# Kernel optimization log

Measured on AMD Instinct MI355X. Metric: run time of the kernel, lower is better.

Reference implementation:

```python
import jax, jax.numpy as jnp
import numpy as np

B, L, V, D = 512, 41, 4, 64        # batch, seq_len=41 (hard-coded in source), vocab=DNA, d_model=64
NL, DI, N, DTR, K = 3, 128, 16, 4, 4  # n_layer, d_inner=2*D, d_state, dt_rank=ceil(D/16), d_conv
NS = 3  # three parallel stacks (layers1/2/3)


def setup_inputs() -> dict:
    key = jax.random.key(0)
    ks = jax.random.split(key, 16)
    s = 0.02
    nrm = lambda k, sh: jax.random.normal(k, sh, jnp.float32) * s
    A_log = jnp.log(jnp.arange(1, N + 1, dtype=jnp.float32))  # S4D-real init
    return {
        "input_ids": jax.random.randint(ks[0], (B, L), 0, V),
        "embedding": nrm(ks[1], (V, D)),
        # per-stack, per-layer Mamba block params, stacked [NS, NL, ...]
        "in_proj": nrm(ks[2], (NS, NL, D, 2 * DI)),
        "conv_w": nrm(ks[3], (NS, NL, DI, 1, K)),
        "conv_b": jnp.zeros((NS, NL, DI), jnp.float32),
        "x_proj": nrm(ks[4], (NS, NL, DI, DTR + 2 * N)),
        "dt_w": nrm(ks[5], (NS, NL, DTR, DI)),
        "dt_b": jnp.full((NS, NL, DI), -2.0, jnp.float32),
        "A_log": jnp.broadcast_to(A_log, (NS, NL, DI, N)) + 0.0,
        "Dp": jnp.ones((NS, NL, DI), jnp.float32),
        "out_proj": nrm(ks[6], (NS, NL, DI, D)),
        "norm_w": jnp.ones((NS, NL, D), jnp.float32),
        "norm_f_w": jnp.ones((D,), jnp.float32),
        "fusion_w": jnp.zeros((NS,), jnp.float32),  # softmax-weighted fusion of the 3 representations
        # LastDense MLP head: 64*41 -> 384 -> 16 -> 1 (dropout is eval-mode identity)
        "W1": nrm(ks[7], (D * L, 384)), "b1": jnp.zeros((384,), jnp.float32),
        "W2": nrm(ks[8], (384, 16)), "b2": jnp.zeros((16,), jnp.float32),
        "W3": nrm(ks[9], (16, 1)), "b3": jnp.zeros((1,), jnp.float32),
    }


def rmsnorm(x, w, eps=1e-5):
    return x * jax.lax.rsqrt(jnp.mean(x * x, axis=-1, keepdims=True) + eps) * w


def silu(x):
    return x * jax.nn.sigmoid(x)


def mamba_block(x, ip, cw, cb, xp, dw, db, al, dp, op):
    # x: [B, L, D]
    bsz = x.shape[0]
    u, res = jnp.split(x @ ip, 2, axis=-1)  # each [B, L, DI]
    # causal depthwise conv1d (torch padding=3 then [..., :L] == left-pad K-1)
    uc = jax.lax.conv_general_dilated(
        u.transpose(0, 2, 1), cw, window_strides=(1,), padding=[(K - 1, 0)],
        feature_group_count=DI, dimension_numbers=("NCH", "OIH", "NCH"))
    u = silu((uc + cb[None, :, None]).transpose(0, 2, 1))  # [B, L, DI]
    dbl = u @ xp  # [B, L, DTR+2N]
    dt = jax.nn.softplus(dbl[..., :DTR] @ dw + db)           # [B, L, DI]
    Bm = dbl[..., DTR:DTR + N]                               # [B, L, N]
    C = dbl[..., DTR + N:]                                   # [B, L, N]
    A = -jnp.exp(al)                                         # [DI, N]
    dA = jnp.exp(dt[..., None] * A)                          # [B, L, DI, N]
    dBu = dt[..., None] * Bm[:, :, None, :] * u[..., None]   # [B, L, DI, N]

    def step(h, xs):
        dA_t, dBu_t, C_t = xs
        h = dA_t * h + dBu_t                                 # [B, DI, N]
        return h, jnp.einsum("bdn,bn->bd", h, C_t)

    h0 = jnp.zeros((bsz, DI, N), x.dtype)
    _, ys = jax.lax.scan(step, h0, (dA.transpose(1, 0, 2, 3), dBu.transpose(1, 0, 2, 3), C.transpose(1, 0, 2)))
    y = ys.transpose(1, 0, 2) + u * dp                       # [B, L, DI]
    return (y * silu(res)) @ op                              # [B, L, D]


def _forward(input_ids, embedding, in_proj, conv_w, conv_b, x_proj, dt_w, dt_b,
             A_log, Dp, out_proj, norm_w, norm_f_w, fusion_w, W1, b1, W2, b2, W3, b3):
    emb = embedding[input_ids]  # [B, L, D]

    def run_stack(ip, cw, cb, xp, dw, db, al, dp, op, nw):
        x = emb
        for i in range(NL):  # residual: x + MambaBlock(RMSNorm(x))
            x = x + mamba_block(rmsnorm(x, nw[i]), ip[i], cw[i], cb[i], xp[i], dw[i], db[i], al[i], dp[i], op[i])
        return x

    stack_out = jax.vmap(run_stack)(in_proj, conv_w, conv_b, x_proj, dt_w, dt_b,
                                    A_log, Dp, out_proj, norm_w)  # [NS, B, L, D]
    stack_out = rmsnorm(stack_out, norm_f_w)  # final norm_f per stack
    fused = jnp.einsum("s,sbld->bld", jax.nn.softmax(fusion_w), stack_out)  # fusion of 3 reps
    flat = fused.reshape(fused.shape[0], L * D)
    h = jax.nn.relu(flat @ W1 + b1)
    h = jax.nn.relu(h @ W2 + b2)
    logits = (h @ W3 + b3)[:, 0]
    return jax.nn.sigmoid(logits)  # [B]


def reference(input_ids, embedding, in_proj, conv_w, conv_b, x_proj, dt_w, dt_b,
              A_log, Dp, out_proj, norm_w, norm_f_w, fusion_w, W1, b1, W2, b2, W3, b3):
    return _forward(input_ids, embedding, in_proj, conv_w, conv_b, x_proj, dt_w, dt_b,
                    A_log, Dp, out_proj, norm_w, norm_f_w, fusion_w, W1, b1, W2, b2, W3, b3)
```

## Files before the change

### kernel.cpp

```cpp
#include <hip/hip_runtime.h>
#include <hip/hip_bf16.h>
#include <math.h>

#define Bq  512
#define Lq  41
#define Vq  4
#define Dq  64
#define NLq 3
#define DIq 128
#define Nq  16
#define DTRq 4
#define Kq  4
#define NSq 3
#define H1q 384
#define H2q 16
#define FLATq (Lq*Dq)

typedef __attribute__((ext_vector_type(8))) short frag8;
typedef __attribute__((ext_vector_type(4))) float f32x4;

__device__ __forceinline__ float b2f(unsigned short u) {
    union { float f; unsigned int i; } v; v.i = ((unsigned int)u) << 16; return v.f;
}
__device__ __forceinline__ unsigned short f2b_rne(float f) {
    union { float f; unsigned int i; } v; v.f = f;
    unsigned int x = v.i;
    return (unsigned short)((x + 0x7fffu + ((x >> 16) & 1u)) >> 16);
}
__device__ __forceinline__ unsigned short f2b_tr(float f) {
    union { float f; unsigned int i; } v; v.f = f;
    return (unsigned short)(v.i >> 16);
}
__device__ __forceinline__ float fast_rcp(float x) { return __builtin_amdgcn_rcpf(x); }

__global__ __launch_bounds__(256) void prep_kernel(const float* __restrict__ W1,
                                                   const float* __restrict__ in_proj,
                                                   const float* __restrict__ x_proj,
                                                   const float* __restrict__ out_proj,
                                                   unsigned short* __restrict__ W1b,
                                                   unsigned short* __restrict__ Wb_in,
                                                   unsigned short* __restrict__ xp_b,
                                                   unsigned short* __restrict__ op_b) {
    const int bx = blockIdx.x;
    if (bx < 246) {
        __shared__ float t[64][65];
        const int k0 = (bx / 6) * 64, n0 = (bx % 6) * 64;
        for (int idx = threadIdx.x; idx < 4096; idx += 256) {
            int kr = idx >> 6, nc = idx & 63;
            t[kr][nc] = W1[(size_t)(k0 + kr) * H1q + n0 + nc];
        }
        __syncthreads();
        for (int idx = threadIdx.x; idx < 4096; idx += 256) {
            int nr = idx >> 6, kc = idx & 63;
            W1b[(size_t)(n0 + nr) * FLATq + k0 + kc] = f2b_rne(t[kc][nr]);
        }
        return;
    }
    int idx = (bx - 246) * 256 + threadIdx.x;
    if (idx < 9*256*64) {
        int sl = idx >> 14, rem = idx & 16383;
        int n = rem >> 6, k = rem & 63;
        Wb_in[idx] = f2b_rne(in_proj[(size_t)sl*16384 + k*256 + n]);
    } else if (idx < 9*256*64 + 9*48*128) {
        int i2 = idx - 9*256*64;
        int sl = i2 / 6144, rem = i2 % 6144;
        int c = rem >> 7, k = rem & 127;
        float v = (c < 36) ? x_proj[(size_t)sl*(128*36) + k*36 + c] : 0.f;
        xp_b[i2] = f2b_rne(v);
    } else if (idx < 9*256*64 + 9*48*128 + 9*64*128) {
        int i3 = idx - (9*256*64 + 9*48*128);
        int sl = i3 >> 13, rem = i3 & 8191;
        int n = rem >> 7, k = rem & 127;
        op_b[i3] = f2b_rne(out_proj[(size_t)sl*8192 + k*64 + n]);
    }
}

__global__ __launch_bounds__(256, 4) void mamba_stack(
    unsigned short* __restrict__ Xn,
    const int* __restrict__ ids,
    const float* __restrict__ emb,
    const unsigned short* __restrict__ Wb_in,
    const float* __restrict__ conv_w,
    const float* __restrict__ conv_b,
    const unsigned short* __restrict__ xp_b,
    const float* __restrict__ dt_w,
    const float* __restrict__ dt_b,
    const float* __restrict__ A_log,
    const float* __restrict__ Dp,
    const unsigned short* __restrict__ op_b,
    const float* __restrict__ norm_w,
    const float* __restrict__ norm_f_w,
    const float* __restrict__ fusion_w)
{
    const int b = blockIdx.x, s = blockIdx.y, tid = threadIdx.x;
    const int wave = tid >> 6, lane = tid & 63;
    const int nl = lane & 15, quad = lane >> 4;

    __shared__ float          xt  [Lq][64];
    __shared__ unsigned short u_lb[48][136];
    __shared__ unsigned short rs_lb[Lq][128];
    __shared__ __align__(16) char un_buf[6912];
    unsigned short (*xn_lb)[72] = (unsigned short(*)[72])un_buf;
    float          (*dbl_s)[40] = (float(*)[40])un_buf;

    for (int l = wave; l < Lq; l += 4) {
        int id = ids[b * Lq + l];
        xt[l][lane] = emb[id * Dq + lane];
    }

    for (int layer = 0; layer < NLq; ++layer) {
        const int sl = s * NLq + layer;

        {
            const float nwv = norm_w[(size_t)sl * Dq + lane];
            for (int l = wave; l < 48; l += 4) {
                if (l < Lq) {
                    float v  = xt[l][lane];
                    float ss = v * v;
                    #pragma unroll
                    for (int off = 32; off; off >>= 1) ss += __shfl_xor(ss, off, 64);
                    float scale = __builtin_amdgcn_rsqf(ss * (1.0f / Dq) + 1e-5f);
                    xn_lb[l][lane] = f2b_tr(v * scale * nwv);
                } else {
                    xn_lb[l][lane] = 0;
                }
            }
        }
        __syncthreads();

        {
            #pragma unroll
            for (int t = 0; t < 12; ++t) {
                const int id = wave * 12 + t;
                const int mt = id >> 4, nt = id & 15;
                const unsigned short* Wp = Wb_in + ((size_t)(sl * 256 + nt * 16 + nl)) * 64 + quad * 8;
                frag8 a0 = *(const frag8*)&xn_lb[mt * 16 + nl][quad * 8];
                frag8 a1 = *(const frag8*)&xn_lb[mt * 16 + nl][32 + quad * 8];
                frag8 b0 = *(const frag8*)&Wp[0];
                frag8 b1 = *(const frag8*)&Wp[32];
                f32x4 c = {0.f, 0.f, 0.f, 0.f};
                c = __builtin_amdgcn_mfma_f32_16x16x32_bf16(a0, b0, c, 0, 0, 0);
                c = __builtin_amdgcn_mfma_f32_16x16x32_bf16(a1, b1, c, 0, 0, 0);
                const int col = nt * 16 + nl;
                const int r0 = mt * 16 + quad * 4;
                if (col < DIq) {
                    #pragma unroll
                    for (int r = 0; r < 4; ++r) u_lb[r0 + r][col] = f2b_tr(c[r]);
                } else {
                    const int d = col - DIq;
                    #pragma unroll
                    for (int r = 0; r < 4; ++r) {
                        int row = r0 + r;
                        if (row < Lq) {
                            float v = c[r];
                            rs_lb[row][d] = f2b_tr(v * fast_rcp(1.f + __expf(-v)));
                        }
                    }
                }
            }
        }
        __syncthreads();

        {
            const float* cw = conv_w + (size_t)sl * (DIq * Kq);
            const int d = tid >> 1, half = tid & 1;
            const float c0 = cw[d*4+0], c1 = cw[d*4+1], c2 = cw[d*4+2], c3 = cw[d*4+3];
            const float cbv = conv_b[(size_t)sl * DIq + d];
            float w0 = 0.f, w1 = 0.f, w2 = 0.f;
            if (half) { w0 = b2f(u_lb[18][d]); w1 = b2f(u_lb[19][d]); w2 = b2f(u_lb[20][d]); }
            const int base = half ? 21 : 0;
            const int cnt  = half ? 20 : 21;
            for (int i = 0; i < cnt; ++i) {
                int l = base + i;
                float cur = b2f(u_lb[l][d]);
                float a = fmaf(w0, c0, fmaf(w1, c1, fmaf(w2, c2, fmaf(cur, c3, cbv))));
                u_lb[l][d] = f2b_tr(a * fast_rcp(1.f + __expf(-a)));
                w0 = w1; w1 = w2; w2 = cur;
            }
        }
        __syncthreads();

        {
            for (int t = wave; t < 9; t += 4) {
                const int mt = t / 3, ct = t % 3;
                f32x4 c = {0.f, 0.f, 0.f, 0.f};
                #pragma unroll
                for (int kt = 0; kt < 4; ++kt) {
                    frag8 a  = *(const frag8*)&u_lb[mt * 16 + nl][kt * 32 + quad * 8];
                    frag8 bb = *(const frag8*)&xp_b[((size_t)(sl * 48 + ct * 16 + nl)) * 128 + kt * 32 + quad * 8];
                    c = __builtin_amdgcn_mfma_f32_16x16x32_bf16(a, bb, c, 0, 0, 0);
                }
                const int col = ct * 16 + nl, r0 = mt * 16 + quad * 4;
                if (col < 40) {
                    #pragma unroll
                    for (int r = 0; r < 4; ++r) {
                        int row = r0 + r;
                        if (row < Lq) dbl_s[row][col] = c[r];
                    }
                }
            }
        }
        __syncthreads();

        {
            const int d = tid >> 1, half = tid & 1;
            const float* al = A_log + (size_t)sl * (DIq * Nq) + d * Nq + half * 8;
            float A2[8], h[8];
            #pragma unroll
            for (int n = 0; n < 8; ++n) {
                A2[n] = -__expf(al[n]) * 1.442695041f;
                h[n] = 0.f;
            }
            const float* dw = dt_w + (size_t)sl * (DTRq * DIq);
            const float dw0 = dw[d], dw1 = dw[DIq + d], dw2 = dw[2*DIq + d], dw3 = dw[3*DIq + d];
            const float dbv = dt_b[(size_t)sl * DIq + d];
            const float dpd = Dp[(size_t)sl * DIq + d];
            for (int l = 0; l < Lq; ++l) {
                float4 q0 = *(const float4*)&dbl_s[l][0];
                float x  = fmaf(q0.x, dw0, fmaf(q0.y, dw1, fmaf(q0.z, dw2, fmaf(q0.w, dw3, dbv))));
                float dt_ = fmaxf(x, 0.f) + __logf(1.f + __expf(-fabsf(x)));
                float u_  = b2f(u_lb[l][d]);
                float rsv = b2f(rs_lb[l][d]);
                float4 B0 = *(const float4*)&dbl_s[l][4  + half * 8];
                float4 B1 = *(const float4*)&dbl_s[l][8  + half * 8];
                float4 C0 = *(const float4*)&dbl_s[l][20 + half * 8];
                float4 C1 = *(const float4*)&dbl_s[l][24 + half * 8];
                float dtu = dt_ * u_;
                float Bv[8] = {B0.x,B0.y,B0.z,B0.w,B1.x,B1.y,B1.z,B1.w};
                float Cv[8] = {C0.x,C0.y,C0.z,C0.w,C1.x,C1.y,C1.z,C1.w};
                float y = 0.f;
                #pragma unroll
                for (int n = 0; n < 8; ++n) {
                    float dA = __builtin_amdgcn_exp2f(dt_ * A2[n]);
                    h[n] = fmaf(dA, h[n], Bv[n] * dtu);
                    y    = fmaf(h[n], Cv[n], y);
                }
                y += __shfl_xor(y, 1, 64);
                if (!half) u_lb[l][d] = f2b_tr(fmaf(u_, dpd, y) * rsv);
            }
        }
        __syncthreads();

        {
            const int ntG = wave;
            for (int mt = 0; mt < 3; ++mt) {
                f32x4 c = {0.f, 0.f, 0.f, 0.f};
                #pragma unroll
                for (int kt = 0; kt < 4; ++kt) {
                    frag8 a  = *(const frag8*)&u_lb[mt * 16 + nl][kt * 32 + quad * 8];
                    frag8 bb = *(const frag8*)&op_b[((size_t)(sl * 64 + ntG * 16 + nl)) * 128 + kt * 32 + quad * 8];
                    c = __builtin_amdgcn_mfma_f32_16x16x32_bf16(a, bb, c, 0, 0, 0);
                }
                const int j = ntG * 16 + nl, r0 = mt * 16 + quad * 4;
                #pragma unroll
                for (int r = 0; r < 4; ++r) {
                    int row = r0 + r;
                    if (row < Lq) xt[row][j] += c[r];
                }
            }
        }
        __syncthreads();
    }

    {
        float fw0 = fusion_w[0], fw1 = fusion_w[1], fw2 = fusion_w[2];
        float mx = fmaxf(fw0, fmaxf(fw1, fw2));
        float e0 = __expf(fw0 - mx), e1 = __expf(fw1 - mx), e2 = __expf(fw2 - mx);
        float sw = (s == 0 ? e0 : (s == 1 ? e1 : e2)) * fast_rcp(e0 + e1 + e2);
        float nf = norm_f_w[lane] * sw;
        unsigned short* xr = Xn + ((size_t)s * Bq + b) * FLATq;
        for (int l = wave; l < Lq; l += 4) {
            float v  = xt[l][lane];
            float ss = v * v;
            #pragma unroll
            for (int off = 32; off; off >>= 1) ss += __shfl_xor(ss, off, 64);
            float scale = __builtin_amdgcn_rsqf(ss * (1.0f / Dq) + 1e-5f);
            xr[l * Dq + lane] = f2b_tr(v * scale * nf);
        }
    }
}

__global__ __launch_bounds__(256) void head_gemm1(const unsigned short* __restrict__ Xn,
                                                  const unsigned short* __restrict__ W1b,
                                                  const float* __restrict__ b1,
                                                  float* __restrict__ H1) {
    const int tid = threadIdx.x;
    const int wave = tid >> 6, lane = tid & 63;
    const int nl = lane & 15, quad = lane >> 4;
    const int mt = blockIdx.x, nt = blockIdx.y;

    __shared__ float red[4][16][17];

    const int kbeg = (wave < 2) ? wave * 21 : 42 + (wave - 2) * 20;
    const int kcnt = (wave < 2) ? 21 : 20;
    const size_t SB = (size_t)Bq * FLATq;
    const unsigned short* A0 = Xn  + (size_t)(mt * 16 + nl) * FLATq + quad * 8;
    const unsigned short* Br = W1b + (size_t)(nt * 16 + nl) * FLATq + quad * 8;

    f32x4 c = {0.f, 0.f, 0.f, 0.f};
    for (int ks = kbeg; ks < kbeg + kcnt; ++ks) {
        const int off = ks * 32;
        frag8 bb = *(const frag8*)(Br + off);
        frag8 a0 = *(const frag8*)(A0 + off);
        frag8 a1 = *(const frag8*)(A0 + SB + off);
        frag8 a2 = *(const frag8*)(A0 + 2 * SB + off);
        c = __builtin_amdgcn_mfma_f32_16x16x32_bf16(a0, bb, c, 0, 0, 0);
        c = __builtin_amdgcn_mfma_f32_16x16x32_bf16(a1, bb, c, 0, 0, 0);
        c = __builtin_amdgcn_mfma_f32_16x16x32_bf16(a2, bb, c, 0, 0, 0);
    }
    #pragma unroll
    for (int r = 0; r < 4; ++r) red[wave][quad * 4 + r][nl] = c[r];
    __syncthreads();

    const int row = tid >> 4, colv = tid & 15;
    float acc = red[0][row][colv] + red[1][row][colv]
              + red[2][row][colv] + red[3][row][colv];
    const int col = nt * 16 + colv;
    H1[(size_t)(mt * 16 + row) * H1q + col] = fmaxf(acc + b1[col], 0.f);
}

__global__ __launch_bounds__(256) void head_final(const float* __restrict__ H1,
                                                  const float* __restrict__ W2,
                                                  const float* __restrict__ b2,
                                                  const float* __restrict__ W3,
                                                  const float* __restrict__ b3,
                                                  float* __restrict__ out) {
    const int b0 = blockIdx.x * 16, tid = threadIdx.x;
    __shared__ float H1s[16 * H1q];
    __shared__ float h2s[16][16];
    for (int idx = tid; idx < 16 * H1q; idx += 256)
        H1s[idx] = H1[(size_t)b0 * H1q + idx];
    __syncthreads();
    {
        const int row = tid >> 4, g = tid & 15;
        float acc = b2[g];
        for (int k = 0; k < H1q; ++k)
            acc = fmaf(H1s[row * H1q + k], W2[k * H2q + g], acc);
        h2s[row][g] = fmaxf(acc, 0.f);
    }
    __syncthreads();
    if (tid < 16) {
        float z = b3[0];
        #pragma unroll
        for (int k = 0; k < H2q; ++k) z = fmaf(h2s[tid][k], W3[k], z);
        out[b0 + tid] = fast_rcp(1.f + __expf(-z));
    }
}

extern "C" void kernel_launch(void* const* d_in, const int* in_sizes, int n_in,
                              void* d_out, int out_size, void* d_ws, size_t ws_size,
                              hipStream_t stream) {
    const int*   ids      = (const int*)  d_in[0];
    const float* emb      = (const float*)d_in[1];
    const float* in_proj  = (const float*)d_in[2];
    const float* conv_w   = (const float*)d_in[3];
    const float* conv_b   = (const float*)d_in[4];
    const float* x_proj   = (const float*)d_in[5];
    const float* dt_w     = (const float*)d_in[6];
    const float* dt_b     = (const float*)d_in[7];
    const float* A_log    = (const float*)d_in[8];
    const float* Dp       = (const float*)d_in[9];
    const float* out_proj = (const float*)d_in[10];
    const float* norm_w   = (const float*)d_in[11];
    const float* norm_f_w = (const float*)d_in[12];
    const float* fusion_w = (const float*)d_in[13];
    const float* W1       = (const float*)d_in[14];
    const float* b1       = (const float*)d_in[15];
    const float* W2       = (const float*)d_in[16];
    const float* b2       = (const float*)d_in[17];
    const float* W3       = (const float*)d_in[18];
    const float* b3       = (const float*)d_in[19];
    float* out = (float*)d_out;

    unsigned short* Xn    = (unsigned short*)d_ws;
    unsigned short* Wb_in = Xn    + (size_t)NSq * Bq * FLATq;
    unsigned short* xp_b  = Wb_in + 9*256*64;
    unsigned short* op_b  = xp_b  + 9*48*128;
    unsigned short* W1b   = op_b  + 9*64*128;
    float*          H1    = (float*)(W1b + (size_t)H1q * FLATq);

    hipLaunchKernelGGL(prep_kernel, dim3(246 + 1080), dim3(256), 0, stream,
                       W1, in_proj, x_proj, out_proj, W1b, Wb_in, xp_b, op_b);

    hipLaunchKernelGGL(mamba_stack, dim3(Bq, NSq), dim3(256), 0, stream,
                       Xn, ids, emb, Wb_in, conv_w, conv_b, xp_b, dt_w, dt_b,
                       A_log, Dp, op_b, norm_w, norm_f_w, fusion_w);

    hipLaunchKernelGGL(head_gemm1, dim3(Bq/16, H1q/64), dim3(256), 0, stream,
                       Xn, W1b, b1, H1);

    hipLaunchKernelGGL(head_final, dim3(Bq/16), dim3(256), 0, stream,
                       H1, W2, b2, W3, b3, out);
}
```

Measured before the change: 313.1 us.

## Use geometric dA recurrence when A is arithmetic, shrink LDS, pair softplus

A new prep block checks per layer whether the A values form an arithmetic sequence and stores a flag. When it is set, the scan computes dA with two exp2 calls plus multiplies instead of eight exp2 calls per step. The two lanes of each pair also split the softplus of consecutive rows and exchange results by shuffle. LDS buffers are trimmed to 41 rows, with clamped A-row indices and guarded stores, which lowers shared memory per block and may allow higher occupancy. The fast path is chosen at runtime and falls back to the general path, but the repeated multiplies accumulate slightly more rounding error.

Measured after the change: 316.5 us. Within noise of the previous version (+1.1%).

```diff
diff --git a/kernel.cpp b/kernel.cpp
--- a/kernel.cpp
+++ b/kernel.cpp
@@ -37,10 +37,12 @@
                                                    const float* __restrict__ in_proj,
                                                    const float* __restrict__ x_proj,
                                                    const float* __restrict__ out_proj,
+                                                   const float* __restrict__ A_log,
                                                    unsigned short* __restrict__ W1b,
                                                    unsigned short* __restrict__ Wb_in,
                                                    unsigned short* __restrict__ xp_b,
-                                                   unsigned short* __restrict__ op_b) {
+                                                   unsigned short* __restrict__ op_b,
+                                                   int* __restrict__ Aflag) {
     const int bx = blockIdx.x;
     if (bx < 246) {
         __shared__ float t[64][65];
@@ -53,6 +55,26 @@
         for (int idx = threadIdx.x; idx < 4096; idx += 256) {
             int nr = idx >> 6, kc = idx & 63;
             W1b[(size_t)(n0 + nr) * FLATq + k0 + kc] = f2b_rne(t[kc][nr]);
+        }
+        return;
+    }
+    if (bx == 246 + 1080) {
+        const int tid = threadIdx.x;
+        const int d = tid >> 1, half = tid & 1;
+        for (int sl = 0; sl < 9; ++sl) {
+            const float* al = A_log + (size_t)sl * (DIq * Nq) + d * Nq + half * 8;
+            float A2[8];
+            #pragma unroll
+            for (int n = 0; n < 8; ++n) A2[n] = -__expf(al[n]);
+            float d0 = A2[1] - A2[0];
+            int ok = 1;
+            #pragma unroll
+            for (int n = 2; n < 8; ++n) {
+                float dk = A2[n] - A2[n-1];
+                if (!(fabsf(dk - d0) <= 1e-4f * fabsf(d0) + 1e-12f)) ok = 0;
+            }
+            int allok = __syncthreads_and(ok);
+            if (tid == 0) Aflag[sl] = allok;
         }
         return;
     }
@@ -90,16 +112,17 @@
     const unsigned short* __restrict__ op_b,
     const float* __restrict__ norm_w,
     const float* __restrict__ norm_f_w,
-    const float* __restrict__ fusion_w)
+    const float* __restrict__ fusion_w,
+    const int* __restrict__ Aflag)
 {
     const int b = blockIdx.x, s = blockIdx.y, tid = threadIdx.x;
     const int wave = tid >> 6, lane = tid & 63;
     const int nl = lane & 15, quad = lane >> 4;
 
     __shared__ float          xt  [Lq][64];
-    __shared__ unsigned short u_lb[48][136];
-    __shared__ unsigned short rs_lb[Lq][128];
-    __shared__ __align__(16) char un_buf[6912];
+    __shared__ unsigned short u_lb[Lq][136];
+    __shared__ unsigned short rs_lb[Lq][132];
+    __shared__ __align__(16) char un_buf[6560];
     unsigned short (*xn_lb)[72] = (unsigned short(*)[72])un_buf;
     float          (*dbl_s)[40] = (float(*)[40])un_buf;
 
@@ -113,17 +136,13 @@
 
         {
             const float nwv = norm_w[(size_t)sl * Dq + lane];
-            for (int l = wave; l < 48; l += 4) {
-                if (l < Lq) {
-                    float v  = xt[l][lane];
-                    float ss = v * v;
-                    #pragma unroll
-                    for (int off = 32; off; off >>= 1) ss += __shfl_xor(ss, off, 64);
-                    float scale = __builtin_amdgcn_rsqf(ss * (1.0f / Dq) + 1e-5f);
-                    xn_lb[l][lane] = f2b_tr(v * scale * nwv);
-                } else {
-                    xn_lb[l][lane] = 0;
-                }
+            for (int l = wave; l < Lq; l += 4) {
+                float v  = xt[l][lane];
+                float ss = v * v;
+                #pragma unroll
+                for (int off = 32; off; off >>= 1) ss += __shfl_xor(ss, off, 64);
+                float scale = __builtin_amdgcn_rsqf(ss * (1.0f / Dq) + 1e-5f);
+                xn_lb[l][lane] = f2b_tr(v * scale * nwv);
             }
         }
         __syncthreads();
@@ -133,9 +152,10 @@
             for (int t = 0; t < 12; ++t) {
                 const int id = wave * 12 + t;
                 const int mt = id >> 4, nt = id & 15;
+                int ar = mt * 16 + nl; if (ar > Lq - 1) ar = Lq - 1;
                 const unsigned short* Wp = Wb_in + ((size_t)(sl * 256 + nt * 16 + nl)) * 64 + quad * 8;
-                frag8 a0 = *(const frag8*)&xn_lb[mt * 16 + nl][quad * 8];
-                frag8 a1 = *(const frag8*)&xn_lb[mt * 16 + nl][32 + quad * 8];
+                frag8 a0 = *(const frag8*)&xn_lb[ar][quad * 8];
+                frag8 a1 = *(const frag8*)&xn_lb[ar][32 + quad * 8];
                 frag8 b0 = *(const frag8*)&Wp[0];
                 frag8 b1 = *(const frag8*)&Wp[32];
                 f32x4 c = {0.f, 0.f, 0.f, 0.f};
@@ -145,7 +165,10 @@
                 const int r0 = mt * 16 + quad * 4;
                 if (col < DIq) {
                     #pragma unroll
-                    for (int r = 0; r < 4; ++r) u_lb[r0 + r][col] = f2b_tr(c[r]);
+                    for (int r = 0; r < 4; ++r) {
+                        int row = r0 + r;
+                        if (row < Lq) u_lb[row][col] = f2b_tr(c[r]);
+                    }
                 } else {
                     const int d = col - DIq;
                     #pragma unroll
@@ -183,10 +206,11 @@
         {
             for (int t = wave; t < 9; t += 4) {
                 const int mt = t / 3, ct = t % 3;
+                int ar = mt * 16 + nl; if (ar > Lq - 1) ar = Lq - 1;
                 f32x4 c = {0.f, 0.f, 0.f, 0.f};
                 #pragma unroll
                 for (int kt = 0; kt < 4; ++kt) {
-                    frag8 a  = *(const frag8*)&u_lb[mt * 16 + nl][kt * 32 + quad * 8];
+                    frag8 a  = *(const frag8*)&u_lb[ar][kt * 32 + quad * 8];
                     frag8 bb = *(const frag8*)&xp_b[((size_t)(sl * 48 + ct * 16 + nl)) * 128 + kt * 32 + quad * 8];
                     c = __builtin_amdgcn_mfma_f32_16x16x32_bf16(a, bb, c, 0, 0, 0);
                 }
@@ -211,16 +235,20 @@
                 A2[n] = -__expf(al[n]) * 1.442695041f;
                 h[n] = 0.f;
             }
+            const float dd = A2[1] - A2[0];
+            const bool fastA = __builtin_amdgcn_readfirstlane(Aflag[sl]) != 0;
             const float* dw = dt_w + (size_t)sl * (DTRq * DIq);
             const float dw0 = dw[d], dw1 = dw[DIq + d], dw2 = dw[2*DIq + d], dw3 = dw[3*DIq + d];
             const float dbv = dt_b[(size_t)sl * DIq + d];
             const float dpd = Dp[(size_t)sl * DIq + d];
-            for (int l = 0; l < Lq; ++l) {
+
+            auto softplus_row = [&](int l) -> float {
                 float4 q0 = *(const float4*)&dbl_s[l][0];
-                float x  = fmaf(q0.x, dw0, fmaf(q0.y, dw1, fmaf(q0.z, dw2, fmaf(q0.w, dw3, dbv))));
-                float dt_ = fmaxf(x, 0.f) + __logf(1.f + __expf(-fabsf(x)));
+                float x = fmaf(q0.x, dw0, fmaf(q0.y, dw1, fmaf(q0.z, dw2, fmaf(q0.w, dw3, dbv))));
+                return fmaxf(x, 0.f) + __logf(1.f + __expf(-fabsf(x)));
+            };
+            auto step = [&](int l, float dt_) {
                 float u_  = b2f(u_lb[l][d]);
-                float rsv = b2f(rs_lb[l][d]);
                 float4 B0 = *(const float4*)&dbl_s[l][4  + half * 8];
                 float4 B1 = *(const float4*)&dbl_s[l][8  + half * 8];
                 float4 C0 = *(const float4*)&dbl_s[l][20 + half * 8];
@@ -228,26 +256,49 @@
                 float dtu = dt_ * u_;
                 float Bv[8] = {B0.x,B0.y,B0.z,B0.w,B1.x,B1.y,B1.z,B1.w};
                 float Cv[8] = {C0.x,C0.y,C0.z,C0.w,C1.x,C1.y,C1.z,C1.w};
+                float dA[8];
+                if (fastA) {
+                    dA[0] = __builtin_amdgcn_exp2f(dt_ * A2[0]);
+                    float r = __builtin_amdgcn_exp2f(dt_ * dd);
+                    #pragma unroll
+                    for (int n = 1; n < 8; ++n) dA[n] = dA[n-1] * r;
+                } else {
+                    #pragma unroll
+                    for (int n = 0; n < 8; ++n) dA[n] = __builtin_amdgcn_exp2f(dt_ * A2[n]);
+                }
                 float y = 0.f;
                 #pragma unroll
                 for (int n = 0; n < 8; ++n) {
-                    float dA = __builtin_amdgcn_exp2f(dt_ * A2[n]);
-                    h[n] = fmaf(dA, h[n], Bv[n] * dtu);
+                    h[n] = fmaf(dA[n], h[n], Bv[n] * dtu);
                     y    = fmaf(h[n], Cv[n], y);
                 }
                 y += __shfl_xor(y, 1, 64);
-                if (!half) u_lb[l][d] = f2b_tr(fmaf(u_, dpd, y) * rsv);
-            }
+                if (!half) {
+                    float rsv = b2f(rs_lb[l][d]);
+                    u_lb[l][d] = f2b_tr(fmaf(u_, dpd, y) * rsv);
+                }
+            };
+
+            for (int l0 = 0; l0 + 1 < Lq; l0 += 2) {
+                float dts = softplus_row(l0 + half);
+                float dto = __shfl_xor(dts, 1, 64);
+                float dtA = half ? dto : dts;
+                float dtB = half ? dts : dto;
+                step(l0, dtA);
+                step(l0 + 1, dtB);
+            }
+            step(Lq - 1, softplus_row(Lq - 1));
         }
         __syncthreads();
 
         {
             const int ntG = wave;
             for (int mt = 0; mt < 3; ++mt) {
+                int ar = mt * 16 + nl; if (ar > Lq - 1) ar = Lq - 1;
                 f32x4 c = {0.f, 0.f, 0.f, 0.f};
                 #pragma unroll
                 for (int kt = 0; kt < 4; ++kt) {
-                    frag8 a  = *(const frag8*)&u_lb[mt * 16 + nl][kt * 32 + quad * 8];
+                    frag8 a  = *(const frag8*)&u_lb[ar][kt * 32 + quad * 8];
                     frag8 bb = *(const frag8*)&op_b[((size_t)(sl * 64 + ntG * 16 + nl)) * 128 + kt * 32 + quad * 8];
                     c = __builtin_amdgcn_mfma_f32_16x16x32_bf16(a, bb, c, 0, 0, 0);
                 }
@@ -378,13 +429,14 @@
     unsigned short* op_b  = xp_b  + 9*48*128;
     unsigned short* W1b   = op_b  + 9*64*128;
     float*          H1    = (float*)(W1b + (size_t)H1q * FLATq);
-
-    hipLaunchKernelGGL(prep_kernel, dim3(246 + 1080), dim3(256), 0, stream,
-                       W1, in_proj, x_proj, out_proj, W1b, Wb_in, xp_b, op_b);
+    int*            Aflag = (int*)H1;
+
+    hipLaunchKernelGGL(prep_kernel, dim3(246 + 1080 + 1), dim3(256), 0, stream,
+                       W1, in_proj, x_proj, out_proj, A_log, W1b, Wb_in, xp_b, op_b, Aflag);
 
     hipLaunchKernelGGL(mamba_stack, dim3(Bq, NSq), dim3(256), 0, stream,
                        Xn, ids, emb, Wb_in, conv_w, conv_b, xp_b, dt_w, dt_b,
-                       A_log, Dp, op_b, norm_w, norm_f_w, fusion_w);
+                       A_log, Dp, op_b, norm_w, norm_f_w, fusion_w, Aflag);
 
     hipLaunchKernelGGL(head_gemm1, dim3(Bq/16, H1q/64), dim3(256), 0, stream,
                        Xn, W1b, b1, H1);
```
